# Kernel optimization log

Measured on AMD Instinct MI355X. Metric: run time of the kernel, lower is better.

The kernel has to match this reference:

```python
import jax, jax.numpy as jnp
import numpy as np
from jax import lax

B, C_IN, H_IN, W_IN = 32, 3, 128, 128
MID = 64
FINAL_HW = 13  # 128 ->conv 126 ->pool 62 ->conv 60 ->pool 29 ->conv 27 ->pool 13
EPS_SN = 1e-12
EPS_BN = 1e-5


def _norm(x):
    return x / jnp.maximum(jnp.linalg.norm(x), EPS_SN)


def setup_inputs() -> dict:
    key = jax.random.key(0)
    ks = jax.random.split(key, 10)
    x = jax.random.normal(ks[0], (B, C_IN, H_IN, W_IN), jnp.float32)
    w0 = jax.random.normal(ks[1], (MID, C_IN, 1, 1), jnp.float32) * 0.1
    w1 = jax.random.normal(ks[2], (MID, MID, 3, 3), jnp.float32) * 0.05
    w2 = jax.random.normal(ks[3], (MID, MID, 3, 3), jnp.float32) * 0.05
    w3 = jax.random.normal(ks[4], (MID, MID, 3, 3), jnp.float32) * 0.05
    gamma = jnp.ones((4, MID), jnp.float32)
    beta = jnp.zeros((4, MID), jnp.float32)
    # torch inits weight to zero / bias to identity; use small random weight so theta varies
    W_reg = jax.random.normal(ks[5], (6, MID * FINAL_HW * FINAL_HW), jnp.float32) * 0.01
    b_reg = jnp.array([1, 0, 0, 0, 1, 0], jnp.float32)
    u0 = _norm(jax.random.normal(ks[6], (2,), jnp.float32))
    v0 = _norm(jax.random.normal(ks[7], (3,), jnp.float32))
    return dict(x=x, w0=w0, w1=w1, w2=w2, w3=w3, gamma=gamma, beta=beta,
                W_reg=W_reg, b_reg=b_reg, u0=u0, v0=v0)


def reference(x, w0, w1, w2, w3, gamma, beta, W_reg, b_reg, u0, v0):
    conv = lambda h, w: lax.conv_general_dilated(
        h, w, (1, 1), 'VALID', dimension_numbers=('NCHW', 'OIHW', 'NCHW'))

    def bn_relu(h, g, b):  # BatchNorm2d in training mode (batch statistics)
        m = h.mean(axis=(0, 2, 3), keepdims=True)
        v = h.var(axis=(0, 2, 3), keepdims=True)
        return jax.nn.relu((h - m) / jnp.sqrt(v + EPS_BN) * g[None, :, None, None]
                           + b[None, :, None, None])

    def pool(h):  # MaxPool2d(kernel=3, stride=2)
        return lax.reduce_window(h, -jnp.inf, lax.max,
                                 (1, 1, 3, 3), (1, 1, 2, 2), 'VALID')

    # localization CNN
    h = bn_relu(conv(x, w0), gamma[0], beta[0])
    for i, wk in enumerate((w1, w2, w3)):
        h = bn_relu(pool(conv(h, wk)), gamma[i + 1], beta[i + 1])

    flat = h.reshape(h.shape[0], -1)
    theta = (flat @ W_reg.T + b_reg).reshape(-1, 2, 3)  # (B,2,3)

    # per-sample spectral normalization with u,v carried sequentially across batch
    def sample_step(carry, Wm):
        def power(c, _):
            u, v = c
            v = _norm(Wm.T @ u)
            u = _norm(Wm @ v)
            return (u, v), None
        (u, v), _ = lax.scan(power, carry, None, length=4)
        sigma = u @ (Wm @ v)
        return (u, v), Wm / sigma
    _, theta = lax.scan(sample_step, (u0, v0), theta)

    # affine_grid, align_corners=False
    N, Cc, Hh, Ww = x.shape
    xs = (2 * jnp.arange(Ww, dtype=x.dtype) + 1) / Ww - 1
    ys = (2 * jnp.arange(Hh, dtype=x.dtype) + 1) / Hh - 1
    base = jnp.stack([jnp.tile(xs[None, :], (Hh, 1)),
                      jnp.tile(ys[:, None], (1, Ww)),
                      jnp.ones((Hh, Ww), x.dtype)], axis=-1)  # (H,W,3)
    grid = jnp.einsum('nij,hwj->nhwi', theta, base)  # [...,0]=x, [...,1]=y

    # grid_sample: bilinear, padding_mode='reflection', align_corners=False
    ix = ((grid[..., 0] + 1) * Ww - 1) / 2
    iy = ((grid[..., 1] + 1) * Hh - 1) / 2

    def reflect(c, size):
        lo = -0.5
        span = jnp.asarray(size, c.dtype)
        r = jnp.mod(jnp.abs(c - lo), 2 * span)
        c = jnp.where(r > span, 2 * span - r, r) + lo
        return jnp.clip(c, 0.0, size - 1)

    ix = reflect(ix, Ww)
    iy = reflect(iy, Hh)
    x0 = jnp.floor(ix)
    y0 = jnp.floor(iy)
    wx = (ix - x0)[..., None]
    wy = (iy - y0)[..., None]
    x0i = jnp.clip(x0.astype(jnp.int32), 0, Ww - 1)
    x1i = jnp.clip(x0i + 1, 0, Ww - 1)
    y0i = jnp.clip(y0.astype(jnp.int32), 0, Hh - 1)
    y1i = jnp.clip(y0i + 1, 0, Hh - 1)
    bidx = jnp.arange(N)[:, None, None]
    g = lambda yy, xx: x[bidx, :, yy, xx]  # (N,H,W,C)
    out = (g(y0i, x0i) * (1 - wx) * (1 - wy) + g(y0i, x1i) * wx * (1 - wy)
           + g(y1i, x0i) * (1 - wx) * wy + g(y1i, x1i) * wx * wy)
    return out.transpose(0, 3, 1, 2)  # (N,C,H,W)
```

## Files before the change

kernel.cpp:

```cpp
#include <hip/hip_runtime.h>
#include <math.h>


typedef _Float16 half8_t __attribute__((ext_vector_type(8)));
typedef __fp16 fp16x2 __attribute__((ext_vector_type(2)));
typedef float f32x4 __attribute__((ext_vector_type(4)));

__global__ __launch_bounds__(256) void k_prep(const float* __restrict__ w1,
                                              const float* __restrict__ w2,
                                              const float* __restrict__ w3,
                                              _Float16* __restrict__ Wp,
                                              float* __restrict__ zb) {
  int blk = blockIdx.x;
  if (blk >= 432) {
    int i = (blk - 432) * 256 + threadIdx.x;
    if (i < 400) zb[i] = 0.f;
    return;
  }
  int layer = blk / 144;
  const float* w = (layer == 0) ? w1 : (layer == 1) ? w2 : w3;
  _Float16* W = Wp + (size_t)layer * 73728;
  int i = (blk % 144) * 256 + threadIdx.x;
  int s = i >> 12, rem = i & 4095;
  int ci = rem >> 6, co = rem & 63;
  float wv = w[(co * 64 + ci) * 9 + s];
  _Float16 hi = (_Float16)wv;
  _Float16 lo = (_Float16)((wv - (float)hi) * 2048.0f);
  int g = ci >> 3, e = ci & 7;
  W[(((size_t)(s * 2 + 0) * 8 + g) * 64 + co) * 8 + e] = hi;
  W[(((size_t)(s * 2 + 1) * 8 + g) * 64 + co) * 8 + e] = lo;
}

__global__ __launch_bounds__(256) void k_xstats(const float* __restrict__ x,
                                                float* __restrict__ xst) {
  int g0 = blockIdx.x * 256 + threadIdx.x;
  float a[9] = {0,0,0,0,0,0,0,0,0};
  for (int g = g0; g < 524288; g += 1024 * 256) {
    int b = g >> 14, p = g & 16383;
    const float* xb = x + (size_t)b * 49152 + p;
    float x0 = xb[0], x1 = xb[16384], x2 = xb[32768];
    a[0] += x0; a[1] += x1; a[2] += x2;
    a[3] += x0 * x0; a[4] += x0 * x1; a[5] += x0 * x2;
    a[6] += x1 * x1; a[7] += x1 * x2; a[8] += x2 * x2;
  }
  __shared__ float red[256];
  for (int k = 0; k < 9; ++k) {
    red[threadIdx.x] = a[k];
    __syncthreads();
    for (int s = 128; s > 0; s >>= 1) {
      if (threadIdx.x < s) red[threadIdx.x] += red[threadIdx.x + s];
      __syncthreads();
    }
    if (threadIdx.x == 0) atomicAdd(&xst[k], red[0]);
    __syncthreads();
  }
}

__global__ void k_bn0(const float* __restrict__ xst, const float* __restrict__ w0,
                      const float* __restrict__ gamma, const float* __restrict__ beta,
                      float* __restrict__ sb0) {
  int c = threadIdx.x;
  if (c >= 64) return;
  const float invN = 1.f / 524288.f;
  float mu0 = xst[0] * invN, mu1 = xst[1] * invN, mu2 = xst[2] * invN;
  float M00 = xst[3] * invN, M01 = xst[4] * invN, M02 = xst[5] * invN;
  float M11 = xst[6] * invN, M12 = xst[7] * invN, M22 = xst[8] * invN;
  float wa = w0[c * 3], wb = w0[c * 3 + 1], wc = w0[c * 3 + 2];
  float m  = wa * mu0 + wb * mu1 + wc * mu2;
  float e2 = wa * wa * M00 + wb * wb * M11 + wc * wc * M22
           + 2.f * (wa * wb * M01 + wa * wc * M02 + wb * wc * M12);
  float var = e2 - m * m;
  float sc = gamma[c] / sqrtf(var + 1e-5f);
  sb0[2 * c] = sc;
  sb0[2 * c + 1] = beta[c] - m * sc;
}

__global__ __launch_bounds__(256) void k_conv1_mfma(
    const float* __restrict__ x, const float* __restrict__ w0,
    const _Float16* __restrict__ Wp, const float* __restrict__ sb0,
    float* __restrict__ out) {
  __shared__ __align__(16) unsigned char smem[51488];
  float* x_lds = (float*)(smem + 47520);

  int bid = blockIdx.x;
  int cb = bid & 1, pr = (bid >> 1) % 62, b = (bid >> 1) / 62;
  int CB = cb * 62;
  int t = threadIdx.x;
  int lane = t & 63, wv = t >> 6;
  int cwv = wv * 16;
  int l15 = lane & 15, l4 = lane >> 4;

  for (int i = t; i < 990; i += 256) {
    int ch = i / 330, pos = i - ch * 330;
    int ir = pos / 66, ic = pos - ir * 66;
    x_lds[ch * 330 + pos] =
        x[((size_t)(b * 3 + ch) << 14) + (2 * pr + ir) * 128 + CB + ic];
  }

  f32x4 acc1[3][4], acc2[3][4];
  #pragma unroll
  for (int r = 0; r < 3; ++r)
    #pragma unroll
    for (int ct = 0; ct < 4; ++ct) {
      acc1[r][ct] = (f32x4)0.f;
      acc2[r][ct] = (f32x4)0.f;
    }

  int pair = t & 15;
  int posb = t >> 4;
  int LB = l15 * 144 + l4 * 16;

  for (int q = 0; q < 2; ++q) {
    int ci0 = q * 32 + 2 * pair, ci1 = ci0 + 1;
    float w00 = w0[ci0*3], w01 = w0[ci0*3+1], w02 = w0[ci0*3+2];
    float w10 = w0[ci1*3], w11 = w0[ci1*3+1], w12 = w0[ci1*3+2];
    float sc0 = sb0[2*ci0], bi0 = sb0[2*ci0+1];
    float sc1 = sb0[2*ci1], bi1 = sb0[2*ci1+1];
    __syncthreads();
    for (int pos = posb; pos < 330; pos += 16) {
      float x0 = x_lds[pos], x1 = x_lds[330 + pos], x2 = x_lds[660 + pos];
      float v0 = fmaxf(fmaf(fmaf(x2, w02, fmaf(x1, w01, x0 * w00)), sc0, bi0), 0.f);
      float v1 = fmaxf(fmaf(fmaf(x2, w12, fmaf(x1, w11, x0 * w10)), sc1, bi1), 0.f);
      fp16x2 hv = __builtin_amdgcn_cvt_pkrtz(v0, v1);
      float l0 = (v0 - (float)hv[0]) * 2048.f;
      float l1 = (v1 - (float)hv[1]) * 2048.f;
      fp16x2 lv = __builtin_amdgcn_cvt_pkrtz(l0, l1);
      int base = pos * 144 + pair * 4;
      *(fp16x2*)(smem + base) = hv;
      *(fp16x2*)(smem + base + 64) = lv;
    }
    __syncthreads();

    #pragma unroll
    for (int s = 0; s < 9; ++s) {
      const int kh = s / 3, kw = s % 3;
      half8_t Ah[4], Al[4];
      #pragma unroll
      for (int ct = 0; ct < 4; ++ct) {
        Ah[ct] = *(const half8_t*)(Wp + ((size_t)((s*2+0)*8 + q*4 + l4) * 64 + ct*16 + l15) * 8);
        Al[ct] = *(const half8_t*)(Wp + ((size_t)((s*2+1)*8 + q*4 + l4) * 64 + ct*16 + l15) * 8);
      }
      #pragma unroll
      for (int r = 0; r < 3; ++r) {
        int rowoff = ((r + kh) * 66 + cwv + kw) * 144 + LB;
        half8_t Bh = *(const half8_t*)(smem + rowoff);
        half8_t Bl = *(const half8_t*)(smem + rowoff + 64);
        #pragma unroll
        for (int ct = 0; ct < 4; ++ct) {
          acc1[r][ct] = __builtin_amdgcn_mfma_f32_16x16x32_f16(Ah[ct], Bh, acc1[r][ct], 0, 0, 0);
          acc2[r][ct] = __builtin_amdgcn_mfma_f32_16x16x32_f16(Ah[ct], Bl, acc2[r][ct], 0, 0, 0);
          acc2[r][ct] = __builtin_amdgcn_mfma_f32_16x16x32_f16(Al[ct], Bh, acc2[r][ct], 0, 0, 0);
        }
      }
    }
  }

  __syncthreads();
  float* ctile = (float*)smem;
  #pragma unroll
  for (int r = 0; r < 3; ++r)
    #pragma unroll
    for (int ct = 0; ct < 4; ++ct)
      #pragma unroll
      for (int e = 0; e < 4; ++e) {
        int co = ct * 16 + l4 * 4 + e;
        ctile[(co * 3 + r) * 65 + cwv + l15] =
            acc1[r][ct][e] + acc2[r][ct][e] * (1.f / 2048.f);
      }
  __syncthreads();
  for (int i = t; i < 64 * 31; i += 256) {
    int co = i / 31, pcl = i - co * 31;
    float m = -INFINITY;
    #pragma unroll
    for (int dr = 0; dr < 3; ++dr)
      #pragma unroll
      for (int dc = 0; dc < 3; ++dc)
        m = fmaxf(m, ctile[(co * 3 + dr) * 65 + 2 * pcl + dc]);
    out[((size_t)(b * 64 + co) * 62 + pr) * 62 + cb * 31 + pcl] = m;
  }
}

template<int IN, int POOLW, int NH>
__global__ __launch_bounds__(256) void k_convpool_mfma(
    const float* __restrict__ in, const _Float16* __restrict__ Wp,
    const float* __restrict__ sb, float* __restrict__ out) {
  __shared__ __align__(16) unsigned char smem[25344];

  int bid = blockIdx.x;
  int h  = (NH == 2) ? (bid & 1) : 0;
  int pw = (NH == 2) ? (bid >> 1) : bid;
  int pr = pw % POOLW;
  int b  = pw / POOLW;
  int CB = h * 30;
  int t = threadIdx.x;
  int lane = t & 63, wv = t >> 6;
  int l15 = lane & 15, l4 = lane >> 4;
  int wc = wv & 1, wo = wv >> 1;

  f32x4 acc1[3][2], acc2[3][2];
  #pragma unroll
  for (int r = 0; r < 3; ++r)
    #pragma unroll
    for (int c = 0; c < 2; ++c) { acc1[r][c] = (f32x4)0.f; acc2[r][c] = (f32x4)0.f; }

  for (int q = 0; q < 2; ++q) {
    __syncthreads();
    for (int li = t; li < 5440; li += 256) {
      int ci = li / 170, pos = li - ci * 170;
      int ir = pos / 34, ic = pos - ir * 34;
      int gci = q * 32 + ci;
      int gc = CB + ic;
      float v = 0.f;
      if (gc < IN)
        v = fmaxf(fmaf(in[((size_t)(b * 64 + gci) * IN + 2 * pr + ir) * IN + gc],
                       sb[2 * gci], sb[2 * gci + 1]), 0.f);
      _Float16 hi = (_Float16)v;
      _Float16 lo = (_Float16)((v - (float)hi) * 2048.f);
      int base = pos * 144 + ci * 2;
      *(_Float16*)(smem + base) = hi;
      *(_Float16*)(smem + base + 64) = lo;
    }
    __syncthreads();
    #pragma unroll
    for (int s = 0; s < 9; ++s) {
      const int kh = s / 3, kw = s % 3;
      half8_t Ah[2], Al[2];
      #pragma unroll
      for (int cti = 0; cti < 2; ++cti) {
        int co = (wo * 2 + cti) * 16 + l15;
        Ah[cti] = *(const half8_t*)(Wp + ((size_t)((s*2+0)*8 + q*4 + l4) * 64 + co) * 8);
        Al[cti] = *(const half8_t*)(Wp + ((size_t)((s*2+1)*8 + q*4 + l4) * 64 + co) * 8);
      }
      #pragma unroll
      for (int r = 0; r < 3; ++r) {
        int rowoff = ((r + kh) * 34 + wc * 16 + l15 + kw) * 144 + l4 * 16;
        half8_t Bh = *(const half8_t*)(smem + rowoff);
        half8_t Bl = *(const half8_t*)(smem + rowoff + 64);
        #pragma unroll
        for (int cti = 0; cti < 2; ++cti) {
          acc1[r][cti] = __builtin_amdgcn_mfma_f32_16x16x32_f16(Ah[cti], Bh, acc1[r][cti], 0, 0, 0);
          acc2[r][cti] = __builtin_amdgcn_mfma_f32_16x16x32_f16(Ah[cti], Bl, acc2[r][cti], 0, 0, 0);
          acc2[r][cti] = __builtin_amdgcn_mfma_f32_16x16x32_f16(Al[cti], Bh, acc2[r][cti], 0, 0, 0);
        }
      }
    }
  }

  __syncthreads();
  float* ctile = (float*)smem;
  #pragma unroll
  for (int r = 0; r < 3; ++r)
    #pragma unroll
    for (int cti = 0; cti < 2; ++cti)
      #pragma unroll
      for (int e = 0; e < 4; ++e) {
        int co = (wo * 2 + cti) * 16 + l4 * 4 + e;
        ctile[(co * 3 + r) * 33 + wc * 16 + l15] =
            acc1[r][cti][e] + acc2[r][cti][e] * (1.f / 2048.f);
      }
  __syncthreads();
  constexpr int NPC = (NH == 1) ? POOLW : 15;
  int pc0 = h * 15;
  for (int i = t; i < 64 * NPC; i += 256) {
    int co = i / NPC, pcl = i - co * NPC;
    int pc = pc0 + pcl;
    if (pc >= POOLW) continue;
    float m = -INFINITY;
    #pragma unroll
    for (int dr = 0; dr < 3; ++dr)
      #pragma unroll
      for (int dc = 0; dc < 3; ++dc)
        m = fmaxf(m, ctile[(co * 3 + dr) * 33 + 2 * pcl + dc]);
    out[((size_t)(b * 64 + co) * POOLW + pr) * POOLW + pc] = m;
  }
}

__global__ __launch_bounds__(256) void k_stats(const float* __restrict__ h,
                                               float* __restrict__ st, int S) {
  int c = blockIdx.x & 63, b = blockIdx.x >> 6;
  const float* base = h + (size_t)(b * 64 + c) * S;
  float s = 0.f, s2 = 0.f;
  for (int i = threadIdx.x; i < S; i += 256) {
    float v = base[i]; s += v; s2 += v * v;
  }
  __shared__ float r1[256], r2[256];
  r1[threadIdx.x] = s; r2[threadIdx.x] = s2;
  __syncthreads();
  for (int str = 128; str > 0; str >>= 1) {
    if (threadIdx.x < str) {
      r1[threadIdx.x] += r1[threadIdx.x + str];
      r2[threadIdx.x] += r2[threadIdx.x + str];
    }
    __syncthreads();
  }
  if (threadIdx.x == 0) {
    atomicAdd(&st[2 * c],     r1[0]);
    atomicAdd(&st[2 * c + 1], r2[0]);
  }
}

__global__ void k_finalize(const float* __restrict__ st,
                           const float* __restrict__ gamma,
                           const float* __restrict__ beta,
                           float* __restrict__ sb, int layer, float invN) {
  int t = threadIdx.x;
  if (t >= 64) return;
  float m   = st[2 * t] * invN;
  float var = st[2 * t + 1] * invN - m * m;
  float sc  = gamma[layer * 64 + t] / sqrtf(var + 1e-5f);
  sb[2 * t]     = sc;
  sb[2 * t + 1] = beta[layer * 64 + t] - m * sc;
}

__global__ __launch_bounds__(256) void k_theta(const float* __restrict__ h3,
                                               const float* __restrict__ sb3,
                                               const float* __restrict__ Wreg,
                                               const float* __restrict__ breg,
                                               float* __restrict__ theta_raw) {
  int b = blockIdx.x, tid = threadIdx.x;
  float acc[6] = {0.f, 0.f, 0.f, 0.f, 0.f, 0.f};
  const float* hb = h3 + (size_t)b * 10816;
  for (int i = tid; i < 10816; i += 256) {
    int c = i / 169;
    float f = fmaxf(fmaf(hb[i], sb3[2 * c], sb3[2 * c + 1]), 0.f);
    #pragma unroll
    for (int j = 0; j < 6; ++j) acc[j] += f * Wreg[j * 10816 + i];
  }
  __shared__ float red[6][256];
  #pragma unroll
  for (int j = 0; j < 6; ++j) red[j][tid] = acc[j];
  __syncthreads();
  for (int s = 128; s > 0; s >>= 1) {
    if (tid < s) {
      #pragma unroll
      for (int j = 0; j < 6; ++j) red[j][tid] += red[j][tid + s];
    }
    __syncthreads();
  }
  if (tid < 6) theta_raw[b * 6 + tid] = red[tid][0] + breg[tid];
}

__global__ void k_spectral(const float* __restrict__ theta_raw,
                           const float* __restrict__ u0v,
                           const float* __restrict__ v0v,
                           float* __restrict__ theta) {
  if (threadIdx.x != 0 || blockIdx.x != 0) return;
  float ua = u0v[0], ub = u0v[1];
  float va = v0v[0], vb = v0v[1], vc = v0v[2];
  for (int n = 0; n < 32; ++n) {
    float W[6];
    #pragma unroll
    for (int k = 0; k < 6; ++k) W[k] = theta_raw[n * 6 + k];
    #pragma unroll
    for (int it = 0; it < 4; ++it) {
      float t0 = W[0]*ua + W[3]*ub;
      float t1 = W[1]*ua + W[4]*ub;
      float t2 = W[2]*ua + W[5]*ub;
      float nv = fmaxf(sqrtf(t0*t0 + t1*t1 + t2*t2), 1e-12f);
      va = t0/nv; vb = t1/nv; vc = t2/nv;
      float s0 = W[0]*va + W[1]*vb + W[2]*vc;
      float s1 = W[3]*va + W[4]*vb + W[5]*vc;
      float nu = fmaxf(sqrtf(s0*s0 + s1*s1), 1e-12f);
      ua = s0/nu; ub = s1/nu;
    }
    float s0 = W[0]*va + W[1]*vb + W[2]*vc;
    float s1 = W[3]*va + W[4]*vb + W[5]*vc;
    float sigma = ua*s0 + ub*s1;
    #pragma unroll
    for (int k = 0; k < 6; ++k) theta[n * 6 + k] = W[k] / sigma;
  }
}

__global__ __launch_bounds__(256) void k_sample(const float* __restrict__ x,
                                                const float* __restrict__ theta,
                                                float* __restrict__ out) {
  int idx = blockIdx.x * 256 + threadIdx.x;
  int b = idx >> 14, p = idx & 16383;
  int hh = p >> 7, ww = p & 127;
  const float* th = theta + b * 6;
  float xs = (2*ww + 1) * (1.f/128.f) - 1.f;
  float ys = (2*hh + 1) * (1.f/128.f) - 1.f;
  float gx = th[0]*xs + th[1]*ys + th[2];
  float gy = th[3]*xs + th[4]*ys + th[5];
  float ix = ((gx + 1.f) * 128.f - 1.f) * 0.5f;
  float iy = ((gy + 1.f) * 128.f - 1.f) * 0.5f;

  float r;
  r  = fmodf(fabsf(ix + 0.5f), 256.f);
  ix = ((r > 128.f) ? 256.f - r : r) - 0.5f;
  ix = fminf(fmaxf(ix, 0.f), 127.f);
  r  = fmodf(fabsf(iy + 0.5f), 256.f);
  iy = ((r > 128.f) ? 256.f - r : r) - 0.5f;
  iy = fminf(fmaxf(iy, 0.f), 127.f);

  float x0f = floorf(ix), y0f = floorf(iy);
  float wx = ix - x0f, wy = iy - y0f;
  int x0 = (int)x0f; x0 = min(max(x0, 0), 127); int x1 = min(x0 + 1, 127);
  int y0 = (int)y0f; y0 = min(max(y0, 0), 127); int y1 = min(y0 + 1, 127);
  float w00 = (1.f-wx)*(1.f-wy), w10 = wx*(1.f-wy);
  float w01 = (1.f-wx)*wy,       w11 = wx*wy;

  #pragma unroll
  for (int ch = 0; ch < 3; ++ch) {
    const float* xb = x + ((size_t)(b*3 + ch)) * 16384;
    float v = xb[y0*128 + x0]*w00 + xb[y0*128 + x1]*w10
            + xb[y1*128 + x0]*w01 + xb[y1*128 + x1]*w11;
    out[((size_t)(b*3 + ch)) * 16384 + p] = v;
  }
}

extern "C" void kernel_launch(void* const* d_in, const int* in_sizes, int n_in,
                              void* d_out, int out_size, void* d_ws, size_t ws_size,
                              hipStream_t stream) {
  const float* x     = (const float*)d_in[0];
  const float* w0    = (const float*)d_in[1];
  const float* w1    = (const float*)d_in[2];
  const float* w2    = (const float*)d_in[3];
  const float* w3    = (const float*)d_in[4];
  const float* gamma = (const float*)d_in[5];
  const float* beta  = (const float*)d_in[6];
  const float* Wreg  = (const float*)d_in[7];
  const float* breg  = (const float*)d_in[8];
  const float* u0v   = (const float*)d_in[9];
  const float* v0v   = (const float*)d_in[10];
  float* out = (float*)d_out;

  float* ws   = (float*)d_ws;
  float* h1   = ws;
  float* h2   = h1 + 7872512;
  float* h3   = h2 + 1722368;
  float* st   = h3 + 346112;
  float* xst  = st + 384;
  float* sb0  = xst + 16;
  float* sbL  = sb0 + 128;
  float* traw = sbL + 384;
  float* tfin = traw + 192;
  _Float16* Wp = (_Float16*)(tfin + 192);

  k_prep<<<434, 256, 0, stream>>>(w1, w2, w3, Wp, st);
  k_xstats<<<1024, 256, 0, stream>>>(x, xst);
  k_bn0<<<1, 64, 0, stream>>>(xst, w0, gamma, beta, sb0);

  k_conv1_mfma<<<32 * 62 * 2, 256, 0, stream>>>(x, w0, Wp, sb0, h1);
  k_stats<<<2048, 256, 0, stream>>>(h1, st, 3844);
  k_finalize<<<1, 64, 0, stream>>>(st, gamma, beta, sbL, 1, 1.f / 123008.f);

  k_convpool_mfma<62, 29, 2><<<32 * 29 * 2, 256, 0, stream>>>(h1, Wp + 73728, sbL, h2);
  k_stats<<<2048, 256, 0, stream>>>(h2, st + 128, 841);
  k_finalize<<<1, 64, 0, stream>>>(st + 128, gamma, beta, sbL + 128, 2, 1.f / 26912.f);

  k_convpool_mfma<29, 13, 1><<<32 * 13, 256, 0, stream>>>(h2, Wp + 147456, sbL + 128, h3);
  k_stats<<<2048, 256, 0, stream>>>(h3, st + 256, 169);
  k_finalize<<<1, 64, 0, stream>>>(st + 256, gamma, beta, sbL + 256, 3, 1.f / 5408.f);

  k_theta<<<32, 256, 0, stream>>>(h3, sbL + 256, Wreg, breg, traw);
  k_spectral<<<1, 64, 0, stream>>>(traw, u0v, v0v, tfin);
  k_sample<<<2048, 256, 0, stream>>>(x, tfin, out);
}
```

Measured before the change: 582.2 us.

## Fuse BN statistics into conv-pool epilogues and fold finalize into consumers

Each conv+pool kernel now accumulates per-channel sum and sum-of-squares of its pooled outputs in shared-memory atomics and pushes them to global with one atomic per channel per block. This removes the separate stats kernels that re-read every activation tensor. The BN scale/bias finalize and the layer-0 BN computation are folded into the consuming kernels, which drops several tiny launches. The cost is extra shared atomics with contention on the 64 channel slots, redundant per-block finalize math, and a float-atomic accumulation order that is no longer deterministic.

```diff
diff --git a/kernel.cpp b/kernel.cpp
--- a/kernel.cpp
+++ b/kernel.cpp
@@ -56,30 +56,13 @@
   }
 }
 
-__global__ void k_bn0(const float* __restrict__ xst, const float* __restrict__ w0,
-                      const float* __restrict__ gamma, const float* __restrict__ beta,
-                      float* __restrict__ sb0) {
-  int c = threadIdx.x;
-  if (c >= 64) return;
-  const float invN = 1.f / 524288.f;
-  float mu0 = xst[0] * invN, mu1 = xst[1] * invN, mu2 = xst[2] * invN;
-  float M00 = xst[3] * invN, M01 = xst[4] * invN, M02 = xst[5] * invN;
-  float M11 = xst[6] * invN, M12 = xst[7] * invN, M22 = xst[8] * invN;
-  float wa = w0[c * 3], wb = w0[c * 3 + 1], wc = w0[c * 3 + 2];
-  float m  = wa * mu0 + wb * mu1 + wc * mu2;
-  float e2 = wa * wa * M00 + wb * wb * M11 + wc * wc * M22
-           + 2.f * (wa * wb * M01 + wa * wc * M02 + wb * wc * M12);
-  float var = e2 - m * m;
-  float sc = gamma[c] / sqrtf(var + 1e-5f);
-  sb0[2 * c] = sc;
-  sb0[2 * c + 1] = beta[c] - m * sc;
-}
-
 __global__ __launch_bounds__(256) void k_conv1_mfma(
     const float* __restrict__ x, const float* __restrict__ w0,
-    const _Float16* __restrict__ Wp, const float* __restrict__ sb0,
-    float* __restrict__ out) {
+    const _Float16* __restrict__ Wp, const float* __restrict__ xst,
+    const float* __restrict__ gamma, const float* __restrict__ beta,
+    float* __restrict__ out, float* __restrict__ st) {
   __shared__ __align__(16) unsigned char smem[51488];
+  __shared__ float ssum[64], ssq[64];
   float* x_lds = (float*)(smem + 47520);
 
   int bid = blockIdx.x;
@@ -97,6 +80,11 @@
         x[((size_t)(b * 3 + ch) << 14) + (2 * pr + ir) * 128 + CB + ic];
   }
 
+  const float invN0 = 1.f / 524288.f;
+  float mu0 = xst[0]*invN0, mu1 = xst[1]*invN0, mu2 = xst[2]*invN0;
+  float M00 = xst[3]*invN0, M01 = xst[4]*invN0, M02 = xst[5]*invN0;
+  float M11 = xst[6]*invN0, M12 = xst[7]*invN0, M22 = xst[8]*invN0;
+
   f32x4 acc1[3][4], acc2[3][4];
   #pragma unroll
   for (int r = 0; r < 3; ++r)
@@ -114,8 +102,16 @@
     int ci0 = q * 32 + 2 * pair, ci1 = ci0 + 1;
     float w00 = w0[ci0*3], w01 = w0[ci0*3+1], w02 = w0[ci0*3+2];
     float w10 = w0[ci1*3], w11 = w0[ci1*3+1], w12 = w0[ci1*3+2];
-    float sc0 = sb0[2*ci0], bi0 = sb0[2*ci0+1];
-    float sc1 = sb0[2*ci1], bi1 = sb0[2*ci1+1];
+    float m0 = w00*mu0 + w01*mu1 + w02*mu2;
+    float e20 = w00*w00*M00 + w01*w01*M11 + w02*w02*M22
+              + 2.f*(w00*w01*M01 + w00*w02*M02 + w01*w02*M12);
+    float sc0 = gamma[ci0] / sqrtf(e20 - m0*m0 + 1e-5f);
+    float bi0 = beta[ci0] - m0*sc0;
+    float m1 = w10*mu0 + w11*mu1 + w12*mu2;
+    float e21 = w10*w10*M00 + w11*w11*M11 + w12*w12*M22
+              + 2.f*(w10*w11*M01 + w10*w12*M02 + w11*w12*M12);
+    float sc1 = gamma[ci1] / sqrtf(e21 - m1*m1 + 1e-5f);
+    float bi1 = beta[ci1] - m1*sc1;
     __syncthreads();
     for (int pos = posb; pos < 330; pos += 16) {
       float x0 = x_lds[pos], x1 = x_lds[330 + pos], x2 = x_lds[660 + pos];
@@ -167,6 +163,7 @@
         ctile[(co * 3 + r) * 65 + cwv + l15] =
             acc1[r][ct][e] + acc2[r][ct][e] * (1.f / 2048.f);
       }
+  if (t < 64) { ssum[t] = 0.f; ssq[t] = 0.f; }
   __syncthreads();
   for (int i = t; i < 64 * 31; i += 256) {
     int co = i / 31, pcl = i - co * 31;
@@ -176,15 +173,26 @@
       #pragma unroll
       for (int dc = 0; dc < 3; ++dc)
         m = fmaxf(m, ctile[(co * 3 + dr) * 65 + 2 * pcl + dc]);
+    atomicAdd(&ssum[co], m);
+    atomicAdd(&ssq[co], m * m);
     out[((size_t)(b * 64 + co) * 62 + pr) * 62 + cb * 31 + pcl] = m;
+  }
+  __syncthreads();
+  if (t < 64) {
+    atomicAdd(&st[2 * t],     ssum[t]);
+    atomicAdd(&st[2 * t + 1], ssq[t]);
   }
 }
 
 template<int IN, int POOLW, int NH>
 __global__ __launch_bounds__(256) void k_convpool_mfma(
     const float* __restrict__ in, const _Float16* __restrict__ Wp,
-    const float* __restrict__ sb, float* __restrict__ out) {
+    const float* __restrict__ st_in, const float* __restrict__ gamma,
+    const float* __restrict__ beta, int layer, float invN,
+    float* __restrict__ out, float* __restrict__ st_out) {
   __shared__ __align__(16) unsigned char smem[25344];
+  __shared__ float sbl[128];
+  __shared__ float ssum[64], ssq[64];
 
   int bid = blockIdx.x;
   int h  = (NH == 2) ? (bid & 1) : 0;
@@ -197,6 +205,14 @@
   int l15 = lane & 15, l4 = lane >> 4;
   int wc = wv & 1, wo = wv >> 1;
 
+  if (t < 64) {
+    float m = st_in[2 * t] * invN;
+    float var = st_in[2 * t + 1] * invN - m * m;
+    float sc = gamma[layer * 64 + t] / sqrtf(var + 1e-5f);
+    sbl[2 * t] = sc;
+    sbl[2 * t + 1] = beta[layer * 64 + t] - m * sc;
+  }
+
   f32x4 acc1[3][2], acc2[3][2];
   #pragma unroll
   for (int r = 0; r < 3; ++r)
@@ -213,7 +229,7 @@
       float v = 0.f;
       if (gc < IN)
         v = fmaxf(fmaf(in[((size_t)(b * 64 + gci) * IN + 2 * pr + ir) * IN + gc],
-                       sb[2 * gci], sb[2 * gci + 1]), 0.f);
+                       sbl[2 * gci], sbl[2 * gci + 1]), 0.f);
       _Float16 hi = (_Float16)v;
       _Float16 lo = (_Float16)((v - (float)hi) * 2048.f);
       int base = pos * 144 + ci * 2;
@@ -258,6 +274,7 @@
         ctile[(co * 3 + r) * 33 + wc * 16 + l15] =
             acc1[r][cti][e] + acc2[r][cti][e] * (1.f / 2048.f);
       }
+  if (t < 64) { ssum[t] = 0.f; ssq[t] = 0.f; }
   __syncthreads();
   constexpr int NPC = (NH == 1) ? POOLW : 15;
   int pc0 = h * 15;
@@ -271,53 +288,35 @@
       #pragma unroll
       for (int dc = 0; dc < 3; ++dc)
         m = fmaxf(m, ctile[(co * 3 + dr) * 33 + 2 * pcl + dc]);
+    atomicAdd(&ssum[co], m);
+    atomicAdd(&ssq[co], m * m);
     out[((size_t)(b * 64 + co) * POOLW + pr) * POOLW + pc] = m;
   }
-}
-
-__global__ __launch_bounds__(256) void k_stats(const float* __restrict__ h,
-                                               float* __restrict__ st, int S) {
-  int c = blockIdx.x & 63, b = blockIdx.x >> 6;
-  const float* base = h + (size_t)(b * 64 + c) * S;
-  float s = 0.f, s2 = 0.f;
-  for (int i = threadIdx.x; i < S; i += 256) {
-    float v = base[i]; s += v; s2 += v * v;
-  }
-  __shared__ float r1[256], r2[256];
-  r1[threadIdx.x] = s; r2[threadIdx.x] = s2;
-  __syncthreads();
-  for (int str = 128; str > 0; str >>= 1) {
-    if (threadIdx.x < str) {
-      r1[threadIdx.x] += r1[threadIdx.x + str];
-      r2[threadIdx.x] += r2[threadIdx.x + str];
-    }
-    __syncthreads();
-  }
-  if (threadIdx.x == 0) {
-    atomicAdd(&st[2 * c],     r1[0]);
-    atomicAdd(&st[2 * c + 1], r2[0]);
-  }
-}
-
-__global__ void k_finalize(const float* __restrict__ st,
-                           const float* __restrict__ gamma,
-                           const float* __restrict__ beta,
-                           float* __restrict__ sb, int layer, float invN) {
-  int t = threadIdx.x;
-  if (t >= 64) return;
-  float m   = st[2 * t] * invN;
-  float var = st[2 * t + 1] * invN - m * m;
-  float sc  = gamma[layer * 64 + t] / sqrtf(var + 1e-5f);
-  sb[2 * t]     = sc;
-  sb[2 * t + 1] = beta[layer * 64 + t] - m * sc;
+  __syncthreads();
+  if (t < 64) {
+    atomicAdd(&st_out[2 * t],     ssum[t]);
+    atomicAdd(&st_out[2 * t + 1], ssq[t]);
+  }
 }
 
 __global__ __launch_bounds__(256) void k_theta(const float* __restrict__ h3,
-                                               const float* __restrict__ sb3,
+                                               const float* __restrict__ st3,
+                                               const float* __restrict__ gamma,
+                                               const float* __restrict__ beta,
                                                const float* __restrict__ Wreg,
                                                const float* __restrict__ breg,
                                                float* __restrict__ theta_raw) {
   int b = blockIdx.x, tid = threadIdx.x;
+  __shared__ float sb3[128];
+  if (tid < 64) {
+    const float invN = 1.f / 5408.f;
+    float m = st3[2 * tid] * invN;
+    float var = st3[2 * tid + 1] * invN - m * m;
+    float sc = gamma[192 + tid] / sqrtf(var + 1e-5f);
+    sb3[2 * tid] = sc;
+    sb3[2 * tid + 1] = beta[192 + tid] - m * sc;
+  }
+  __syncthreads();
   float acc[6] = {0.f, 0.f, 0.f, 0.f, 0.f, 0.f};
   const float* hb = h3 + (size_t)b * 10816;
   for (int i = tid; i < 10816; i += 256) {
@@ -431,29 +430,22 @@
   float* h3   = h2 + 1722368;
   float* st   = h3 + 346112;
   float* xst  = st + 384;
-  float* sb0  = xst + 16;
-  float* sbL  = sb0 + 128;
-  float* traw = sbL + 384;
+  float* traw = xst + 16;
   float* tfin = traw + 192;
   _Float16* Wp = (_Float16*)(tfin + 192);
 
   k_prep<<<434, 256, 0, stream>>>(w1, w2, w3, Wp, st);
   k_xstats<<<1024, 256, 0, stream>>>(x, xst);
-  k_bn0<<<1, 64, 0, stream>>>(xst, w0, gamma, beta, sb0);
-
-  k_conv1_mfma<<<32 * 62 * 2, 256, 0, stream>>>(x, w0, Wp, sb0, h1);
-  k_stats<<<2048, 256, 0, stream>>>(h1, st, 3844);
-  k_finalize<<<1, 64, 0, stream>>>(st, gamma, beta, sbL, 1, 1.f / 123008.f);
-
-  k_convpool_mfma<62, 29, 2><<<32 * 29 * 2, 256, 0, stream>>>(h1, Wp + 73728, sbL, h2);
-  k_stats<<<2048, 256, 0, stream>>>(h2, st + 128, 841);
-  k_finalize<<<1, 64, 0, stream>>>(st + 128, gamma, beta, sbL + 128, 2, 1.f / 26912.f);
-
-  k_convpool_mfma<29, 13, 1><<<32 * 13, 256, 0, stream>>>(h2, Wp + 147456, sbL + 128, h3);
-  k_stats<<<2048, 256, 0, stream>>>(h3, st + 256, 169);
-  k_finalize<<<1, 64, 0, stream>>>(st + 256, gamma, beta, sbL + 256, 3, 1.f / 5408.f);
-
-  k_theta<<<32, 256, 0, stream>>>(h3, sbL + 256, Wreg, breg, traw);
+
+  k_conv1_mfma<<<32 * 62 * 2, 256, 0, stream>>>(x, w0, Wp, xst, gamma, beta, h1, st);
+
+  k_convpool_mfma<62, 29, 2><<<32 * 29 * 2, 256, 0, stream>>>(
+      h1, Wp + 73728, st, gamma, beta, 1, 1.f / 123008.f, h2, st + 128);
+
+  k_convpool_mfma<29, 13, 1><<<32 * 13, 256, 0, stream>>>(
+      h2, Wp + 147456, st + 128, gamma, beta, 2, 1.f / 26912.f, h3, st + 256);
+
+  k_theta<<<32, 256, 0, stream>>>(h3, st + 256, gamma, beta, Wreg, breg, traw);
   k_spectral<<<1, 64, 0, stream>>>(traw, u0v, v0v, tfin);
   k_sample<<<2048, 256, 0, stream>>>(x, tfin, out);
 }
```

After: 735.0 us. 1.26x slower.
